# Kernel tuning notes

Measured on AMD Instinct MI355X. Metric: run time of the kernel, lower is better.

## Reference

```python
import jax, jax.numpy as jnp
import numpy as np

GROUP = 64      # quantization group size along the K (in_features) dim
QMAX = 7.0      # symmetric signed int4 range [-7, 7]


def fake_quant_w4a4(t):
    """Per-group symmetric int4 fake-quantization along last dim (STE-friendly).

    t: [..., K] with K % GROUP == 0. Emulates nunchaku's quantize_w4a4
    numerics: scale = max|group| / 7, q = clip(round(t/scale)) * scale.
    """
    shp = t.shape
    g = t.reshape(shp[:-1] + (shp[-1] // GROUP, GROUP))
    scale = jnp.maximum(jnp.max(jnp.abs(g), axis=-1, keepdims=True) / QMAX, 1e-8)
    q = jnp.clip(jnp.round(g / scale), -QMAX, QMAX) * scale
    # straight-through estimator so gradients flow through the quant branch
    q = g + jax.lax.stop_gradient(q - g)
    return q.reshape(shp)


def setup_inputs() -> dict:
    key = jax.random.key(0)
    k0, k1, k2, k3, k4, k5 = jax.random.split(key, 6)
    B, K, N, R = 8192, 2048, 2048, 32  # tokens, in_features, out_features, rank
    x = jax.random.normal(k0, (B, K), jnp.float32)
    residual_weight = jax.random.normal(k1, (N, K), jnp.float32) * 0.02
    lora_down = jax.random.normal(k2, (K, R), jnp.float32) * 0.02
    lora_up = jax.random.normal(k3, (N, R), jnp.float32) * 0.02
    smooth = jax.random.uniform(k4, (K,), jnp.float32, minval=0.5, maxval=2.0)
    bias = jax.random.normal(k5, (N,), jnp.float32) * 0.01
    return {"x": x, "residual_weight": residual_weight, "lora_down": lora_down,
            "lora_up": lora_up, "smooth": smooth, "bias": bias}


def reference(x, residual_weight, lora_down, lora_up, smooth, bias):
    """SVDQuant forward: W4A4 GEMM on the residual weight fused with an
    FP low-rank (SVD) correction and per-channel smoothing.

    y = Q4(x*smooth) @ Q4(W_res).T + (x*smooth) @ lora_down @ lora_up.T + bias
    """
    x_s = x * smooth                                   # [B, K] smoothed activations
    y_lr = (x_s @ lora_down) @ lora_up.T               # [B, R] -> [B, N] low-rank branch
    y_q = fake_quant_w4a4(x_s) @ fake_quant_w4a4(residual_weight).T  # int4xint4 branch
    return y_q + y_lr + bias
```

## Files before the change

### kernel.cpp

```cpp
#include <hip/hip_runtime.h>
#include <stdint.h>


typedef __attribute__((ext_vector_type(8))) short short8;
typedef __attribute__((ext_vector_type(8))) unsigned short ushort8;
typedef __attribute__((ext_vector_type(4))) unsigned short ushort4v;
typedef __attribute__((ext_vector_type(4))) float floatx4;

#define M_TOK 8192
#define K_IN  2048
#define N_OUT 2048
#define RANK  32
#define KC    2112
#define XS_STRIDE 2056

__device__ __forceinline__ unsigned short f2bf(float f) {
  unsigned int u = __float_as_uint(f);
  u += 0x7fff + ((u >> 16) & 1);
  return (unsigned short)(u >> 16);
}

__global__ __launch_bounds__(256) void wq_kernel(const float* __restrict__ wgt,
                                                 const float* __restrict__ lup,
                                                 const float* __restrict__ ld,
                                                 unsigned short* __restrict__ Wcat,
                                                 unsigned short* __restrict__ ldT) {
  int row = blockIdx.x, tid = threadIdx.x;
  const float4* wr = (const float4*)(wgt + (size_t)row * K_IN);
  float4 a0 = wr[tid * 2], a1 = wr[tid * 2 + 1];
  float v[8] = {a0.x, a0.y, a0.z, a0.w, a1.x, a1.y, a1.z, a1.w};
  float amax = 0.f;
#pragma unroll
  for (int i = 0; i < 8; ++i) amax = fmaxf(amax, fabsf(v[i]));
  amax = fmaxf(amax, __shfl_xor(amax, 1, 64));
  amax = fmaxf(amax, __shfl_xor(amax, 2, 64));
  amax = fmaxf(amax, __shfl_xor(amax, 4, 64));
  float scale = fmaxf(amax / 7.0f, 1e-8f);
  ushort8 q;
#pragma unroll
  for (int i = 0; i < 8; ++i) {
    float qq = rintf(v[i] / scale);
    qq = fminf(fmaxf(qq, -7.f), 7.f);
    q[i] = f2bf(qq * scale);
  }
  *(ushort8*)(Wcat + (size_t)row * KC + tid * 8) = q;
  if (tid < 32)      Wcat[(size_t)row * KC + 2048 + tid] = f2bf(lup[row * RANK + tid]);
  else if (tid < 64) Wcat[(size_t)row * KC + 2048 + tid] = 0;
  if (row < 256) {
    int i = row * 256 + tid;
    int r = i >> 11, k = i & 2047;
    ldT[r * K_IN + k] = f2bf(ld[k * RANK + r]);
  }
}

__global__ __launch_bounds__(256) void xq_kernel(const float* __restrict__ x,
                                                 const float* __restrict__ smooth,
                                                 const unsigned short* __restrict__ ldT,
                                                 unsigned short* __restrict__ Xcat) {
  __shared__ unsigned short xs[16 * XS_STRIDE];
  __shared__ float red[4][16][32];
  int tid = threadIdx.x;
  int w = tid >> 6, lane = tid & 63, quad = lane >> 4, l16 = lane & 15;
  int rowbase = blockIdx.x * 16;

  {
    int r = tid >> 4, seg = tid & 15;
    const float4* xr = (const float4*)(x + (size_t)(rowbase + r) * K_IN + seg * 128);
    const float4* sr = (const float4*)(smooth + seg * 128);
    unsigned short* xc = Xcat + (size_t)(rowbase + r) * KC + seg * 128;
    unsigned short* xl = xs + r * XS_STRIDE + seg * 128;
#pragma unroll
    for (int g = 0; g < 2; ++g) {
      float v[64];
      float amax = 0.f;
#pragma unroll
      for (int j = 0; j < 16; ++j) {
        float4 a = xr[g * 16 + j];
        float4 s = sr[g * 16 + j];
        v[j * 4 + 0] = a.x * s.x; v[j * 4 + 1] = a.y * s.y;
        v[j * 4 + 2] = a.z * s.z; v[j * 4 + 3] = a.w * s.w;
        amax = fmaxf(amax, fmaxf(fmaxf(fabsf(v[j * 4]), fabsf(v[j * 4 + 1])),
                                 fmaxf(fabsf(v[j * 4 + 2]), fabsf(v[j * 4 + 3]))));
      }
      float scale = fmaxf(amax / 7.0f, 1e-8f);
#pragma unroll
      for (int j = 0; j < 8; ++j) {
        ushort8 q;
#pragma unroll
        for (int t = 0; t < 8; ++t) {
          float qq = rintf(v[j * 8 + t] / scale);
          qq = fminf(fmaxf(qq, -7.f), 7.f);
          q[t] = f2bf(qq * scale);
        }
        *(ushort8*)(xc + g * 64 + j * 8) = q;
        ushort8 sb;
#pragma unroll
        for (int t = 0; t < 8; ++t) sb[t] = f2bf(v[j * 8 + t]);
        *(ushort8*)(xl + g * 64 + j * 8) = sb;
      }
    }
    *(unsigned int*)(Xcat + (size_t)(rowbase + r) * KC + 2080 + seg * 2) = 0u;
  }
  __syncthreads();

  floatx4 acc[2];
  acc[0] = (floatx4)0.f;
  acc[1] = (floatx4)0.f;
  int kbase = w * 512;
#pragma unroll 4
  for (int it = 0; it < 16; ++it) {
    int k = kbase + it * 32 + quad * 8;
    short8 af = *(const short8*)(xs + l16 * XS_STRIDE + k);
    short8 b0 = *(const short8*)(ldT + (size_t)l16 * K_IN + k);
    short8 b1 = *(const short8*)(ldT + (size_t)(16 + l16) * K_IN + k);
    acc[0] = __builtin_amdgcn_mfma_f32_16x16x32_bf16(af, b0, acc[0], 0, 0, 0);
    acc[1] = __builtin_amdgcn_mfma_f32_16x16x32_bf16(af, b1, acc[1], 0, 0, 0);
  }
#pragma unroll
  for (int nt = 0; nt < 2; ++nt)
#pragma unroll
    for (int r = 0; r < 4; ++r)
      red[w][quad * 4 + r][nt * 16 + l16] = acc[nt][r];
  __syncthreads();
  if (tid < 128) {
    int rl = tid >> 3, seg = tid & 7;
    ushort4v o;
#pragma unroll
    for (int j = 0; j < 4; ++j) {
      int c = seg * 4 + j;
      float s = red[0][rl][c] + red[1][rl][c] + red[2][rl][c] + red[3][rl][c];
      o[j] = f2bf(s);
    }
    *(ushort4v*)(Xcat + (size_t)(rowbase + rl) * KC + 2048 + seg * 4) = o;
  }
}

__device__ __forceinline__ void gld_lds16(const unsigned short* g, unsigned short* l) {
  __builtin_amdgcn_global_load_lds(
      (const __attribute__((address_space(1))) unsigned int*)g,
      (__attribute__((address_space(3))) unsigned int*)l, 16, 0, 0);
}

__global__ __launch_bounds__(256) void gemm_kernel(const unsigned short* __restrict__ Xcat,
                                                   const unsigned short* __restrict__ Wcat,
                                                   const float* __restrict__ bias,
                                                   float* __restrict__ out) {
  __shared__ unsigned short smem[16384];
  unsigned short* smemA = smem;
  unsigned short* smemB = smem + 8192;
  int tid = threadIdx.x;
  int w = tid >> 6, lane = tid & 63, quad = lane >> 4, l16 = lane & 15;
  int wm = w >> 1, wn = w & 1;
  int bM = blockIdx.y * 128, bN = blockIdx.x * 128;

  int srow = tid >> 3;
  int cs = (tid & 7) ^ (srow & 7);
  const unsigned short* Ag = Xcat + (size_t)(bM + srow) * KC + cs * 8;
  const unsigned short* Bg = Wcat + (size_t)(bN + srow) * KC + cs * 8;

  int c0 = (quad ^ (l16 & 7)) * 8;
  int c1 = ((4 + quad) ^ (l16 & 7)) * 8;
  int arow[4], brow[4];
#pragma unroll
  for (int mt = 0; mt < 4; ++mt) arow[mt] = (wm * 64 + mt * 16 + l16) * 64;
#pragma unroll
  for (int nt = 0; nt < 4; ++nt) brow[nt] = (wn * 64 + nt * 16 + l16) * 64;

  floatx4 acc[4][4];
#pragma unroll
  for (int mt = 0; mt < 4; ++mt)
#pragma unroll
    for (int nt = 0; nt < 4; ++nt) acc[mt][nt] = (floatx4)0.f;

  for (int kt = 0; kt < 33; ++kt) {
    int k0 = kt * 64;
#pragma unroll
    for (int rd = 0; rd < 4; ++rd) {
      gld_lds16(Ag + (size_t)rd * 32 * KC + k0, smemA + rd * 2048 + w * 512);
      gld_lds16(Bg + (size_t)rd * 32 * KC + k0, smemB + rd * 2048 + w * 512);
    }
    __syncthreads();

    short8 af[4][2], bf[4][2];
#pragma unroll
    for (int mt = 0; mt < 4; ++mt) {
      af[mt][0] = *(const short8*)(smemA + arow[mt] + c0);
      af[mt][1] = *(const short8*)(smemA + arow[mt] + c1);
    }
#pragma unroll
    for (int nt = 0; nt < 4; ++nt) {
      bf[nt][0] = *(const short8*)(smemB + brow[nt] + c0);
      bf[nt][1] = *(const short8*)(smemB + brow[nt] + c1);
    }
#pragma unroll
    for (int kb = 0; kb < 2; ++kb)
#pragma unroll
      for (int mt = 0; mt < 4; ++mt)
#pragma unroll
        for (int nt = 0; nt < 4; ++nt)
          acc[mt][nt] = __builtin_amdgcn_mfma_f32_16x16x32_bf16(af[mt][kb], bf[nt][kb],
                                                                acc[mt][nt], 0, 0, 0);
    __syncthreads();
  }

#pragma unroll
  for (int nt = 0; nt < 4; ++nt) {
    int col = bN + wn * 64 + nt * 16 + l16;
    float bv = bias[col];
#pragma unroll
    for (int mt = 0; mt < 4; ++mt) {
      int row = bM + wm * 64 + mt * 16 + quad * 4;
#pragma unroll
      for (int r = 0; r < 4; ++r)
        out[(size_t)(row + r) * N_OUT + col] = acc[mt][nt][r] + bv;
    }
  }
}

extern "C" void kernel_launch(void* const* d_in, const int* in_sizes, int n_in,
                              void* d_out, int out_size, void* d_ws, size_t ws_size,
                              hipStream_t stream) {
  const float* x      = (const float*)d_in[0];
  const float* wgt    = (const float*)d_in[1];
  const float* ld     = (const float*)d_in[2];
  const float* lup    = (const float*)d_in[3];
  const float* smooth = (const float*)d_in[4];
  const float* bias   = (const float*)d_in[5];
  float* out = (float*)d_out;

  unsigned short* Xcat = (unsigned short*)d_ws;
  unsigned short* Wcat = Xcat + (size_t)M_TOK * KC;
  unsigned short* ldT  = Wcat + (size_t)N_OUT * KC;

  hipLaunchKernelGGL(wq_kernel,   dim3(N_OUT),    dim3(256), 0, stream, wgt, lup, ld, Wcat, ldT);
  hipLaunchKernelGGL(xq_kernel,   dim3(M_TOK/16), dim3(256), 0, stream, x, smooth, ldT, Xcat);
  hipLaunchKernelGGL(gemm_kernel, dim3(N_OUT/128, M_TOK/128), dim3(256), 0, stream,
                     Xcat, Wcat, bias, out);
}
```

Measured before the change: 243.9 us.

## Merge weight and activation quantization into one prep kernel, swizzle GEMM block order

Folds the weight-quant kernel and the activation-quant/low-rank-down kernel into a single launch, with the extra blocks handling the weight rows. The transposed bf16 lora_down buffer is dropped, and lora_down is read directly from fp32 with strided gathers inside the MFMA loop. Activation quantization is restructured so each thread handles 8 contiguous elements per row, with shuffle reductions over the group. The GEMM grid becomes 1D with grouped tile ordering to improve L2 reuse. This saves one launch and a dependency, at the cost of uncoalesced fp32 loads of lora_down repeated in every block.

```diff
diff --git a/kernel.cpp b/kernel.cpp
--- a/kernel.cpp
+++ b/kernel.cpp
@@ -20,15 +20,7 @@
   return (unsigned short)(u >> 16);
 }
 
-__global__ __launch_bounds__(256) void wq_kernel(const float* __restrict__ wgt,
-                                                 const float* __restrict__ lup,
-                                                 const float* __restrict__ ld,
-                                                 unsigned short* __restrict__ Wcat,
-                                                 unsigned short* __restrict__ ldT) {
-  int row = blockIdx.x, tid = threadIdx.x;
-  const float4* wr = (const float4*)(wgt + (size_t)row * K_IN);
-  float4 a0 = wr[tid * 2], a1 = wr[tid * 2 + 1];
-  float v[8] = {a0.x, a0.y, a0.z, a0.w, a1.x, a1.y, a1.z, a1.w};
+__device__ __forceinline__ void quant8(const float* v, unsigned short* q) {
   float amax = 0.f;
 #pragma unroll
   for (int i = 0; i < 8; ++i) amax = fmaxf(amax, fabsf(v[i]));
@@ -36,83 +28,74 @@
   amax = fmaxf(amax, __shfl_xor(amax, 2, 64));
   amax = fmaxf(amax, __shfl_xor(amax, 4, 64));
   float scale = fmaxf(amax / 7.0f, 1e-8f);
-  ushort8 q;
 #pragma unroll
   for (int i = 0; i < 8; ++i) {
     float qq = rintf(v[i] / scale);
     qq = fminf(fmaxf(qq, -7.f), 7.f);
     q[i] = f2bf(qq * scale);
   }
-  *(ushort8*)(Wcat + (size_t)row * KC + tid * 8) = q;
-  if (tid < 32)      Wcat[(size_t)row * KC + 2048 + tid] = f2bf(lup[row * RANK + tid]);
-  else if (tid < 64) Wcat[(size_t)row * KC + 2048 + tid] = 0;
-  if (row < 256) {
-    int i = row * 256 + tid;
-    int r = i >> 11, k = i & 2047;
-    ldT[r * K_IN + k] = f2bf(ld[k * RANK + r]);
-  }
-}
-
-__global__ __launch_bounds__(256) void xq_kernel(const float* __restrict__ x,
-                                                 const float* __restrict__ smooth,
-                                                 const unsigned short* __restrict__ ldT,
-                                                 unsigned short* __restrict__ Xcat) {
+}
+
+__global__ __launch_bounds__(256) void prep_kernel(const float* __restrict__ x,
+                                                   const float* __restrict__ smooth,
+                                                   const float* __restrict__ wgt,
+                                                   const float* __restrict__ ld,
+                                                   const float* __restrict__ lup,
+                                                   unsigned short* __restrict__ Xcat,
+                                                   unsigned short* __restrict__ Wcat) {
   __shared__ unsigned short xs[16 * XS_STRIDE];
   __shared__ float red[4][16][32];
   int tid = threadIdx.x;
+
+  if (blockIdx.x >= 512) {
+    int row = blockIdx.x - 512;
+    const float4* wr = (const float4*)(wgt + (size_t)row * K_IN);
+    float4 a0 = wr[tid * 2], a1 = wr[tid * 2 + 1];
+    float v[8] = {a0.x, a0.y, a0.z, a0.w, a1.x, a1.y, a1.z, a1.w};
+    ushort8 q;
+    quant8(v, (unsigned short*)&q);
+    *(ushort8*)(Wcat + (size_t)row * KC + tid * 8) = q;
+    if (tid < 32)      Wcat[(size_t)row * KC + 2048 + tid] = f2bf(lup[row * RANK + tid]);
+    else if (tid < 64) Wcat[(size_t)row * KC + 2048 + tid] = 0;
+    return;
+  }
+
+  int rowbase = blockIdx.x * 16;
   int w = tid >> 6, lane = tid & 63, quad = lane >> 4, l16 = lane & 15;
-  int rowbase = blockIdx.x * 16;
-
-  {
-    int r = tid >> 4, seg = tid & 15;
-    const float4* xr = (const float4*)(x + (size_t)(rowbase + r) * K_IN + seg * 128);
-    const float4* sr = (const float4*)(smooth + seg * 128);
-    unsigned short* xc = Xcat + (size_t)(rowbase + r) * KC + seg * 128;
-    unsigned short* xl = xs + r * XS_STRIDE + seg * 128;
-#pragma unroll
-    for (int g = 0; g < 2; ++g) {
-      float v[64];
-      float amax = 0.f;
-#pragma unroll
-      for (int j = 0; j < 16; ++j) {
-        float4 a = xr[g * 16 + j];
-        float4 s = sr[g * 16 + j];
-        v[j * 4 + 0] = a.x * s.x; v[j * 4 + 1] = a.y * s.y;
-        v[j * 4 + 2] = a.z * s.z; v[j * 4 + 3] = a.w * s.w;
-        amax = fmaxf(amax, fmaxf(fmaxf(fabsf(v[j * 4]), fabsf(v[j * 4 + 1])),
-                                 fmaxf(fabsf(v[j * 4 + 2]), fabsf(v[j * 4 + 3]))));
-      }
-      float scale = fmaxf(amax / 7.0f, 1e-8f);
-#pragma unroll
-      for (int j = 0; j < 8; ++j) {
-        ushort8 q;
-#pragma unroll
-        for (int t = 0; t < 8; ++t) {
-          float qq = rintf(v[j * 8 + t] / scale);
-          qq = fminf(fmaxf(qq, -7.f), 7.f);
-          q[t] = f2bf(qq * scale);
-        }
-        *(ushort8*)(xc + g * 64 + j * 8) = q;
-        ushort8 sb;
-#pragma unroll
-        for (int t = 0; t < 8; ++t) sb[t] = f2bf(v[j * 8 + t]);
-        *(ushort8*)(xl + g * 64 + j * 8) = sb;
-      }
-    }
-    *(unsigned int*)(Xcat + (size_t)(rowbase + r) * KC + 2080 + seg * 2) = 0u;
-  }
+
+  const float4* sr = (const float4*)smooth;
+  float4 s0 = sr[tid * 2], s1 = sr[tid * 2 + 1];
+#pragma unroll 2
+  for (int r = 0; r < 16; ++r) {
+    const float4* xr = (const float4*)(x + (size_t)(rowbase + r) * K_IN);
+    float4 a0 = xr[tid * 2], a1 = xr[tid * 2 + 1];
+    float v[8] = {a0.x * s0.x, a0.y * s0.y, a0.z * s0.z, a0.w * s0.w,
+                  a1.x * s1.x, a1.y * s1.y, a1.z * s1.z, a1.w * s1.w};
+    ushort8 q;
+    quant8(v, (unsigned short*)&q);
+    *(ushort8*)(Xcat + (size_t)(rowbase + r) * KC + tid * 8) = q;
+    ushort8 sb;
+#pragma unroll
+    for (int t = 0; t < 8; ++t) sb[t] = f2bf(v[t]);
+    *(ushort8*)(xs + r * XS_STRIDE + tid * 8) = sb;
+  }
+  *(unsigned int*)(Xcat + (size_t)(rowbase + (tid >> 4)) * KC + 2080 + (tid & 15) * 2) = 0u;
   __syncthreads();
 
   floatx4 acc[2];
   acc[0] = (floatx4)0.f;
   acc[1] = (floatx4)0.f;
   int kbase = w * 512;
-#pragma unroll 4
+#pragma unroll 2
   for (int it = 0; it < 16; ++it) {
     int k = kbase + it * 32 + quad * 8;
     short8 af = *(const short8*)(xs + l16 * XS_STRIDE + k);
-    short8 b0 = *(const short8*)(ldT + (size_t)l16 * K_IN + k);
-    short8 b1 = *(const short8*)(ldT + (size_t)(16 + l16) * K_IN + k);
+    short8 b0, b1;
+#pragma unroll
+    for (int j = 0; j < 8; ++j) {
+      b0[j] = (short)f2bf(ld[(size_t)(k + j) * RANK + l16]);
+      b1[j] = (short)f2bf(ld[(size_t)(k + j) * RANK + 16 + l16]);
+    }
     acc[0] = __builtin_amdgcn_mfma_f32_16x16x32_bf16(af, b0, acc[0], 0, 0, 0);
     acc[1] = __builtin_amdgcn_mfma_f32_16x16x32_bf16(af, b1, acc[1], 0, 0, 0);
   }
@@ -151,7 +134,11 @@
   int tid = threadIdx.x;
   int w = tid >> 6, lane = tid & 63, quad = lane >> 4, l16 = lane & 15;
   int wm = w >> 1, wn = w & 1;
-  int bM = blockIdx.y * 128, bN = blockIdx.x * 128;
+
+  int bid = blockIdx.x;
+  int g = bid >> 6, r = bid & 63;
+  int bN = (r >> 2) * 128;
+  int bM = (g * 4 + (r & 3)) * 128;
 
   int srow = tid >> 3;
   int cs = (tid & 7) ^ (srow & 7);
@@ -211,8 +198,8 @@
     for (int mt = 0; mt < 4; ++mt) {
       int row = bM + wm * 64 + mt * 16 + quad * 4;
 #pragma unroll
-      for (int r = 0; r < 4; ++r)
-        out[(size_t)(row + r) * N_OUT + col] = acc[mt][nt][r] + bv;
+      for (int r2 = 0; r2 < 4; ++r2)
+        out[(size_t)(row + r2) * N_OUT + col] = acc[mt][nt][r2] + bv;
     }
   }
 }
@@ -230,10 +217,9 @@
 
   unsigned short* Xcat = (unsigned short*)d_ws;
   unsigned short* Wcat = Xcat + (size_t)M_TOK * KC;
-  unsigned short* ldT  = Wcat + (size_t)N_OUT * KC;
-
-  hipLaunchKernelGGL(wq_kernel,   dim3(N_OUT),    dim3(256), 0, stream, wgt, lup, ld, Wcat, ldT);
-  hipLaunchKernelGGL(xq_kernel,   dim3(M_TOK/16), dim3(256), 0, stream, x, smooth, ldT, Xcat);
-  hipLaunchKernelGGL(gemm_kernel, dim3(N_OUT/128, M_TOK/128), dim3(256), 0, stream,
+
+  hipLaunchKernelGGL(prep_kernel, dim3(512 + N_OUT), dim3(256), 0, stream,
+                     x, smooth, wgt, ld, lup, Xcat, Wcat);
+  hipLaunchKernelGGL(gemm_kernel, dim3((N_OUT / 128) * (M_TOK / 128)), dim3(256), 0, stream,
                      Xcat, Wcat, bias, out);
 }
```

Measured after the change: 226.3 us. 1.08x faster.
